# Kernel optimization log

Hardware: AMD Instinct MI355X
Metric: run time of the kernel (lower is better)

The kernel has to match this reference:

```python
import jax, jax.numpy as jnp
import numpy as np

N, E = 50000, 800000
NF, EF, S = 128, 64, 128

def _lin(key, fan_in, fan_out):
    k1, k2 = jax.random.split(key)
    lim = 1.0 / np.sqrt(fan_in)
    W = jax.random.uniform(k1, (fan_in, fan_out), jnp.float32, -lim, lim)
    b = jax.random.uniform(k2, (fan_out,), jnp.float32, -lim, lim)
    return W, b

def setup_inputs() -> dict:
    key = jax.random.key(0)
    ks = jax.random.split(key, 12)
    x = jax.random.normal(ks[0], (N, NF), jnp.float32)
    edge_index = jax.random.randint(ks[1], (2, E), 0, N, jnp.int64)
    edge_attr = jax.random.normal(ks[2], (E, EF), jnp.float32)
    Wn, bn = _lin(ks[3], NF, S)
    We, be = _lin(ks[4], EF, S)
    Wzc, bzc = _lin(ks[5], S, S)   # GCNConv weight/bias (z gate)
    Wzl, bzl = _lin(ks[6], 2 * S, S)
    Wrc, brc = _lin(ks[7], S, S)
    Wrl, brl = _lin(ks[8], 2 * S, S)
    Whc, bhc = _lin(ks[9], S, S)
    Whl, bhl = _lin(ks[10], 2 * S, S)
    Wout, bout = _lin(ks[11], 3 * S, 1)
    return dict(x=x, edge_index=edge_index, edge_attr=edge_attr,
                Wn=Wn, bn=bn, We=We, be=be,
                Wzc=Wzc, bzc=bzc, Wzl=Wzl, bzl=bzl,
                Wrc=Wrc, brc=brc, Wrl=Wrl, brl=brl,
                Whc=Whc, bhc=bhc, Whl=Whl, bhl=bhl,
                Wout=Wout, bout=bout)

def reference(x, edge_index, edge_attr, Wn, bn, We, be,
              Wzc, bzc, Wzl, bzl, Wrc, brc, Wrl, brl,
              Whc, bhc, Whl, bhl, Wout, bout):
    n = x.shape[0]
    src, dst = edge_index[0], edge_index[1]
    xe = jax.nn.relu(x @ Wn + bn)                      # [N,S]
    ea = jax.nn.relu(edge_attr @ We + be)              # [E,S]
    # GCNConv normalization with self-loops (shared across the 3 gates)
    loop = jnp.arange(n)
    s2 = jnp.concatenate([src, loop])
    d2 = jnp.concatenate([dst, loop])
    deg = jax.ops.segment_sum(jnp.ones(s2.shape[0], xe.dtype), d2, n)
    dinv = jax.lax.rsqrt(deg)                          # deg >= 1 (self loops)
    norm = (dinv[s2] * dinv[d2])[:, None]              # [E+N,1]
    def gcn(W, b):
        xw = xe @ W
        return jax.ops.segment_sum(xw[s2] * norm, d2, n) + b
    H = jnp.zeros_like(xe)
    Z = jax.nn.sigmoid(jnp.concatenate([gcn(Wzc, bzc), H], 1) @ Wzl + bzl)
    R = jax.nn.sigmoid(jnp.concatenate([gcn(Wrc, brc), H], 1) @ Wrl + brl)
    Ht = jnp.tanh(jnp.concatenate([gcn(Whc, bhc), H * R], 1) @ Whl + bhl)
    H = Z * H + (1.0 - Z) * Ht                          # [N,S]
    edge_h = jnp.concatenate([H[src], H[dst], ea], axis=1)  # [E,3S]
    return edge_h @ Wout + bout                         # [E,1]
```

## Files before the change

### kernel.cpp

```cpp
#include <hip/hip_runtime.h>
#include <hip/hip_bf16.h>
#include <math.h>

#define NN 50000
#define EE 800000

typedef __bf16 bf16x8 __attribute__((ext_vector_type(8)));
typedef float f32x4 __attribute__((ext_vector_type(4)));

__global__ void k_deg(const int* __restrict__ ei, int* __restrict__ deg) {
    int e = blockIdx.x * 256 + threadIdx.x;
    if (e < EE) atomicAdd(&deg[ei[EE + e]], 1);
}

__global__ void k_wprep(const float* __restrict__ Wzc, const float* __restrict__ bzc,
                        const float* __restrict__ Wzl, const float* __restrict__ bzl,
                        const float* __restrict__ Whc, const float* __restrict__ bhc,
                        const float* __restrict__ Whl, const float* __restrict__ bhl,
                        float* __restrict__ Wcat, float* __restrict__ cb) {
    int i = blockIdx.x;
    int k = threadIdx.x;
    float sz = 0.f, sh = 0.f;
    for (int j = 0; j < 128; j++) {
        sz += Wzc[i * 128 + j] * Wzl[j * 128 + k];
        sh += Whc[i * 128 + j] * Whl[j * 128 + k];
    }
    Wcat[i * 256 + 2 * k]     = sz;
    Wcat[i * 256 + 2 * k + 1] = sh;
    if (i == 0) {
        float bz = bzl[k], bh = bhl[k];
        for (int j = 0; j < 128; j++) {
            bz += bzc[j] * Wzl[j * 128 + k];
            bh += bhc[j] * Whl[j * 128 + k];
        }
        cb[2 * k]     = bz;
        cb[2 * k + 1] = bh;
    }
}

__global__ __launch_bounds__(256) void k_gemm1(const float* __restrict__ A,
                                               const float* __restrict__ B,
                                               const float* __restrict__ bias,
                                               const int* __restrict__ deg,
                                               __hip_bfloat16* __restrict__ C, int M) {
    __shared__ float As[8][128];
    __shared__ float Bs[8][128];
    const int m0 = blockIdx.x * 128;
    const int tid = threadIdx.x;
    const int tx = tid & 15;
    const int ty = tid >> 4;
    float acc[8][8];
#pragma unroll
    for (int i = 0; i < 8; i++)
#pragma unroll
        for (int j = 0; j < 8; j++) acc[i][j] = 0.f;

    for (int k0 = 0; k0 < 128; k0 += 8) {
        {
            int m = tid >> 1, kk = (tid & 1) * 4;
            float4 av = make_float4(0.f, 0.f, 0.f, 0.f);
            if (m0 + m < M) av = *(const float4*)&A[(size_t)(m0 + m) * 128 + k0 + kk];
            As[kk + 0][m] = av.x; As[kk + 1][m] = av.y;
            As[kk + 2][m] = av.z; As[kk + 3][m] = av.w;
        }
        {
            int kb = tid >> 5, n = (tid & 31) * 4;
            float4 bv = *(const float4*)&B[(size_t)(k0 + kb) * 128 + n];
            *(float4*)&Bs[kb][n] = bv;
        }
        __syncthreads();
#pragma unroll
        for (int kk = 0; kk < 8; kk++) {
            float af[8], bf[8];
#pragma unroll
            for (int i = 0; i < 8; i++) af[i] = As[kk][ty + 16 * i];
#pragma unroll
            for (int j = 0; j < 8; j++) bf[j] = Bs[kk][tx + 16 * j];
#pragma unroll
            for (int i = 0; i < 8; i++)
#pragma unroll
                for (int j = 0; j < 8; j++) acc[i][j] += af[i] * bf[j];
        }
        __syncthreads();
    }
#pragma unroll
    for (int i = 0; i < 8; i++) {
        int row = m0 + ty + 16 * i;
        if (row >= M) continue;
        float di = rsqrtf((float)(deg[row] + 1));
#pragma unroll
        for (int j = 0; j < 8; j++) {
            int cg = tx + 16 * j;
            float v = fmaxf(acc[i][j] + bias[cg], 0.f) * di;
            C[(size_t)row * 128 + cg] = __float2bfloat16(v);
        }
    }
}

__global__ __launch_bounds__(256) void k_gemm_gate(const float* __restrict__ A,
                                                   const float* __restrict__ B,
                                                   const float* __restrict__ cb,
                                                   const float* __restrict__ Wout,
                                                   float* __restrict__ aArr,
                                                   float* __restrict__ bArr, int M) {
    __shared__ float As[8][128];
    __shared__ float Bs[8][128];
    const int m0 = blockIdx.x * 128;
    const int n0 = blockIdx.y * 128;
    const int tid = threadIdx.x;
    const int tx = tid & 15;
    const int ty = tid >> 4;
    float acc[8][8];
#pragma unroll
    for (int i = 0; i < 8; i++)
#pragma unroll
        for (int j = 0; j < 8; j++) acc[i][j] = 0.f;

    for (int k0 = 0; k0 < 128; k0 += 8) {
        {
            int m = tid >> 1, kk = (tid & 1) * 4;
            float4 av = make_float4(0.f, 0.f, 0.f, 0.f);
            if (m0 + m < M) av = *(const float4*)&A[(size_t)(m0 + m) * 128 + k0 + kk];
            As[kk + 0][m] = av.x; As[kk + 1][m] = av.y;
            As[kk + 2][m] = av.z; As[kk + 3][m] = av.w;
        }
        {
            int kb = tid >> 5, n = (tid & 31) * 4;
            float4 bv = *(const float4*)&B[(size_t)(k0 + kb) * 256 + n0 + n];
            *(float4*)&Bs[kb][n] = bv;
        }
        __syncthreads();
#pragma unroll
        for (int kk = 0; kk < 8; kk++) {
            float af[8], bf[8];
#pragma unroll
            for (int i = 0; i < 8; i++) af[i] = As[kk][ty + 16 * i];
#pragma unroll
            for (int j = 0; j < 8; j++) bf[j] = Bs[kk][tx + 16 * j];
#pragma unroll
            for (int i = 0; i < 8; i++)
#pragma unroll
                for (int j = 0; j < 8; j++) acc[i][j] += af[i] * bf[j];
        }
        __syncthreads();
    }
#pragma unroll
    for (int i = 0; i < 8; i++) {
        int row = m0 + ty + 16 * i;
        bool live = (row < M);
        float pa = 0.f, pb = 0.f;
#pragma unroll
        for (int j = 0; j < 8; j++) {
            int col = n0 + tx + 16 * j;
            float val = acc[i][j] + cb[col];
            bool odd = (col & 1);
            float s = odd ? tanhf(val) : (1.f / (1.f + expf(-val)));
            float partner = __shfl_xor(s, 1);
            if (!odd) {
                int k = col >> 1;
                float h = (1.f - s) * partner;
                pa += h * Wout[k];
                pb += h * Wout[128 + k];
            }
        }
#pragma unroll
        for (int off = 1; off < 16; off <<= 1) {
            pa += __shfl_xor(pa, off);
            pb += __shfl_xor(pb, off);
        }
        if (live && tx == 0) {
            atomicAdd(&aArr[row], pa);
            atomicAdd(&bArr[row], pb);
        }
    }
}

__global__ void k_scan_a(const int* __restrict__ deg, int* __restrict__ partial) {
    __shared__ int s[256];
    int i = blockIdx.x * 256 + threadIdx.x;
    s[threadIdx.x] = (i < NN) ? deg[i] : 0;
    __syncthreads();
    for (int off = 128; off > 0; off >>= 1) {
        if (threadIdx.x < off) s[threadIdx.x] += s[threadIdx.x + off];
        __syncthreads();
    }
    if (threadIdx.x == 0) partial[blockIdx.x] = s[0];
}

__global__ void k_scan_b(const int* __restrict__ partial, int* __restrict__ partoff, int nb) {
    __shared__ int s[256];
    int v = (threadIdx.x < nb) ? partial[threadIdx.x] : 0;
    s[threadIdx.x] = v;
    __syncthreads();
    for (int off = 1; off < 256; off <<= 1) {
        int t = (threadIdx.x >= off) ? s[threadIdx.x - off] : 0;
        __syncthreads();
        s[threadIdx.x] += t;
        __syncthreads();
    }
    partoff[threadIdx.x] = s[threadIdx.x] - v;
}

__global__ void k_scan_c(const int* __restrict__ deg, const int* __restrict__ partoff,
                         int* __restrict__ rowptr, int* __restrict__ cursor) {
    __shared__ int s[256];
    int i = blockIdx.x * 256 + threadIdx.x;
    int v = (i < NN) ? deg[i] : 0;
    s[threadIdx.x] = v;
    __syncthreads();
    for (int off = 1; off < 256; off <<= 1) {
        int t = (threadIdx.x >= off) ? s[threadIdx.x - off] : 0;
        __syncthreads();
        s[threadIdx.x] += t;
        __syncthreads();
    }
    int excl = s[threadIdx.x] - v + partoff[blockIdx.x];
    if (i < NN) { rowptr[i] = excl; cursor[i] = excl; }
    if (i == 0) rowptr[NN] = EE;
}

__global__ void k_fill(const int* __restrict__ ei, int* __restrict__ cursor,
                       int* __restrict__ col) {
    int e = blockIdx.x * 256 + threadIdx.x;
    if (e < EE) {
        int d = ei[EE + e];
        int p = atomicAdd(&cursor[d], 1);
        col[p] = ei[e];
    }
}

__global__ __launch_bounds__(256) void k_gather(const unsigned int* __restrict__ xsu,
                                                const int* __restrict__ rowptr,
                                                const int* __restrict__ col,
                                                const int* __restrict__ deg,
                                                float* __restrict__ agg) {
    int gt = blockIdx.x * 256 + threadIdx.x;
    int node = gt >> 6;
    int lane = threadIdx.x & 63;
    if (node >= NN) return;
    int beg = rowptr[node], end = rowptr[node + 1];
    unsigned int u = xsu[(size_t)node * 64 + lane];
    float a0 = __uint_as_float(u << 16);
    float a1 = __uint_as_float(u & 0xFFFF0000u);
    int p = beg;
    while (p < end) {
        int rem = end - p;
        int chunk = rem < 64 ? rem : 64;
        int cv = (lane < chunk) ? col[p + lane] : 0;
        int j = 0;
        for (; j + 4 <= chunk; j += 4) {
            int s0 = __shfl(cv, j + 0);
            int s1 = __shfl(cv, j + 1);
            int s2 = __shfl(cv, j + 2);
            int s3 = __shfl(cv, j + 3);
            unsigned int u0 = xsu[(size_t)s0 * 64 + lane];
            unsigned int u1 = xsu[(size_t)s1 * 64 + lane];
            unsigned int u2 = xsu[(size_t)s2 * 64 + lane];
            unsigned int u3 = xsu[(size_t)s3 * 64 + lane];
            a0 += __uint_as_float(u0 << 16) + __uint_as_float(u1 << 16)
                + __uint_as_float(u2 << 16) + __uint_as_float(u3 << 16);
            a1 += __uint_as_float(u0 & 0xFFFF0000u) + __uint_as_float(u1 & 0xFFFF0000u)
                + __uint_as_float(u2 & 0xFFFF0000u) + __uint_as_float(u3 & 0xFFFF0000u);
        }
        for (; j < chunk; j++) {
            int s = __shfl(cv, j);
            unsigned int uv = xsu[(size_t)s * 64 + lane];
            a0 += __uint_as_float(uv << 16);
            a1 += __uint_as_float(uv & 0xFFFF0000u);
        }
        p += 64;
    }
    float di = rsqrtf((float)(deg[node] + 1));
    *(float2*)(agg + (size_t)node * 128 + lane * 2) = make_float2(a0 * di, a1 * di);
}

__global__ __launch_bounds__(256) void k_edge_mfma(const float* __restrict__ EA,
                                                   const int* __restrict__ ei,
                                                   const float* __restrict__ We,
                                                   const float* __restrict__ be,
                                                   const float* __restrict__ Wout,
                                                   const float* __restrict__ boutp,
                                                   const float* __restrict__ aArr,
                                                   const float* __restrict__ bArr,
                                                   float* __restrict__ out) {
    const int lane = threadIdx.x & 63;
    const int ln = lane & 15;
    const int q  = lane >> 4;
    const int wid = (blockIdx.x * 256 + threadIdx.x) >> 6;
    const int nw  = gridDim.x * 4;

    bf16x8 bfrag[2][8];
#pragma unroll
    for (int h = 0; h < 2; h++)
#pragma unroll
        for (int t = 0; t < 8; t++)
#pragma unroll
            for (int j = 0; j < 8; j++)
                bfrag[h][t][j] = (__bf16)We[(h * 32 + q * 8 + j) * 128 + t * 16 + ln];

    float beR[8], w3R[8];
#pragma unroll
    for (int t = 0; t < 8; t++) {
        beR[t] = be[t * 16 + ln];
        w3R[t] = Wout[256 + t * 16 + ln];
    }
    const float b0 = boutp[0];

    for (int tile = wid; tile < EE / 16; tile += nw) {
        const int e0 = tile * 16;
        const float* arow = EA + (size_t)(e0 + ln) * 64;
        float4 v0 = *(const float4*)(arow + q * 8);
        float4 v1 = *(const float4*)(arow + q * 8 + 4);
        float4 v2 = *(const float4*)(arow + 32 + q * 8);
        float4 v3 = *(const float4*)(arow + 32 + q * 8 + 4);
        bf16x8 af0, af1;
        af0[0] = (__bf16)v0.x; af0[1] = (__bf16)v0.y; af0[2] = (__bf16)v0.z; af0[3] = (__bf16)v0.w;
        af0[4] = (__bf16)v1.x; af0[5] = (__bf16)v1.y; af0[6] = (__bf16)v1.z; af0[7] = (__bf16)v1.w;
        af1[0] = (__bf16)v2.x; af1[1] = (__bf16)v2.y; af1[2] = (__bf16)v2.z; af1[3] = (__bf16)v2.w;
        af1[4] = (__bf16)v3.x; af1[5] = (__bf16)v3.y; af1[6] = (__bf16)v3.z; af1[7] = (__bf16)v3.w;

        f32x4 acc[8];
#pragma unroll
        for (int t = 0; t < 8; t++) acc[t] = (f32x4){0.f, 0.f, 0.f, 0.f};
#pragma unroll
        for (int t = 0; t < 8; t++)
            acc[t] = __builtin_amdgcn_mfma_f32_16x16x32_bf16(af0, bfrag[0][t], acc[t], 0, 0, 0);
#pragma unroll
        for (int t = 0; t < 8; t++)
            acc[t] = __builtin_amdgcn_mfma_f32_16x16x32_bf16(af1, bfrag[1][t], acc[t], 0, 0, 0);

        float part[4] = {0.f, 0.f, 0.f, 0.f};
#pragma unroll
        for (int t = 0; t < 8; t++)
#pragma unroll
            for (int r = 0; r < 4; r++) {
                float y = acc[t][r] + beR[t];
                y = fmaxf(y, 0.f);
                part[r] += y * w3R[t];
            }
#pragma unroll
        for (int off = 1; off < 16; off <<= 1) {
#pragma unroll
            for (int r = 0; r < 4; r++) part[r] += __shfl_xor(part[r], off);
        }
        if (ln < 4) {
            float c = (ln == 0) ? part[0] : (ln == 1) ? part[1] : (ln == 2) ? part[2] : part[3];
            int e = e0 + q * 4 + ln;
            out[e] = c + aArr[ei[e]] + bArr[ei[EE + e]] + b0;
        }
    }
}

extern "C" void kernel_launch(void* const* d_in, const int* in_sizes, int n_in,
                              void* d_out, int out_size, void* d_ws, size_t ws_size,
                              hipStream_t stream) {
    const float* x    = (const float*)d_in[0];
    const int*   ei   = (const int*)d_in[1];
    const float* ea   = (const float*)d_in[2];
    const float* Wn   = (const float*)d_in[3];
    const float* bn   = (const float*)d_in[4];
    const float* We   = (const float*)d_in[5];
    const float* be   = (const float*)d_in[6];
    const float* Wzc  = (const float*)d_in[7];
    const float* bzc  = (const float*)d_in[8];
    const float* Wzl  = (const float*)d_in[9];
    const float* bzl  = (const float*)d_in[10];
    const float* Whc  = (const float*)d_in[15];
    const float* bhc  = (const float*)d_in[16];
    const float* Whl  = (const float*)d_in[17];
    const float* bhl  = (const float*)d_in[18];
    const float* Wout = (const float*)d_in[19];
    const float* bout = (const float*)d_in[20];
    float* out = (float*)d_out;

    char* w = (char*)d_ws;
    auto carve = [&](size_t bytes) {
        void* p = (void*)w;
        w += (bytes + 255) / 256 * 256;
        return p;
    };
    __hip_bfloat16* xs = (__hip_bfloat16*)carve((size_t)NN * 128 * 2);
    float* agg     = (float*)carve((size_t)NN * 128 * 4);
    float* Wcat    = (float*)carve(128 * 256 * 4);
    float* cb      = (float*)carve(256 * 4);
    int*   deg     = (int*)carve((size_t)NN * 4);
    int*   rowptr  = (int*)carve((size_t)(NN + 1) * 4);
    int*   cursor  = (int*)carve((size_t)NN * 4);
    int*   col     = (int*)carve((size_t)EE * 4);
    int*   partial = (int*)carve(256 * 4);
    int*   partoff = (int*)carve(256 * 4);
    float* aArr    = (float*)carve((size_t)NN * 4);
    float* bArr    = (float*)carve((size_t)NN * 4);

    hipMemsetAsync(deg, 0, (size_t)NN * 4, stream);
    hipMemsetAsync(aArr, 0, (size_t)NN * 4, stream);
    hipMemsetAsync(bArr, 0, (size_t)NN * 4, stream);
    k_deg<<<(EE + 255) / 256, 256, 0, stream>>>(ei, deg);
    k_wprep<<<128, 128, 0, stream>>>(Wzc, bzc, Wzl, bzl, Whc, bhc, Whl, bhl, Wcat, cb);

    k_gemm1<<<dim3(391, 1), 256, 0, stream>>>(x, Wn, bn, deg, xs, NN);

    const int NB = (NN + 255) / 256;
    k_scan_a<<<NB, 256, 0, stream>>>(deg, partial);
    k_scan_b<<<1, 256, 0, stream>>>(partial, partoff, NB);
    k_scan_c<<<NB, 256, 0, stream>>>(deg, partoff, rowptr, cursor);
    k_fill<<<(EE + 255) / 256, 256, 0, stream>>>(ei, cursor, col);

    k_gather<<<(NN * 64 + 255) / 256, 256, 0, stream>>>((const unsigned int*)xs, rowptr, col, deg, agg);

    k_gemm_gate<<<dim3(391, 2), 256, 0, stream>>>(agg, Wcat, cb, Wout, aArr, bArr, NN);

    k_edge_mfma<<<2048, 256, 0, stream>>>(ea, ei, We, be, Wout, bout, aArr, bArr, out);
}
```

Before: 631.1 us.

## Replace FP32 SIMT GEMMs with bf16 MFMA kernels and store aggregate as bf16

Rewrites the node embedding GEMM and the gate GEMM as wave-level bf16 MFMA kernels that keep weight fragments in registers and loop over 16-row tiles. The gather kernel now writes its aggregate in packed bf16 rather than fp32, which halves that buffer's traffic and lets the gate kernel load MFMA operands directly. The goal is to cut the FP32 FMA cost of the two dense GEMMs, at the price of bf16 rounding on x and on the aggregated features.

```diff
diff --git a/kernel.cpp b/kernel.cpp
--- a/kernel.cpp
+++ b/kernel.cpp
@@ -7,6 +7,7 @@
 
 typedef __bf16 bf16x8 __attribute__((ext_vector_type(8)));
 typedef float f32x4 __attribute__((ext_vector_type(4)));
+typedef unsigned int u32x4 __attribute__((ext_vector_type(4)));
 
 __global__ void k_deg(const int* __restrict__ ei, int* __restrict__ deg) {
     int e = blockIdx.x * 256 + threadIdx.x;
@@ -38,139 +39,148 @@
     }
 }
 
-__global__ __launch_bounds__(256) void k_gemm1(const float* __restrict__ A,
-                                               const float* __restrict__ B,
-                                               const float* __restrict__ bias,
-                                               const int* __restrict__ deg,
-                                               __hip_bfloat16* __restrict__ C, int M) {
-    __shared__ float As[8][128];
-    __shared__ float Bs[8][128];
-    const int m0 = blockIdx.x * 128;
-    const int tid = threadIdx.x;
-    const int tx = tid & 15;
-    const int ty = tid >> 4;
-    float acc[8][8];
-#pragma unroll
-    for (int i = 0; i < 8; i++)
-#pragma unroll
-        for (int j = 0; j < 8; j++) acc[i][j] = 0.f;
-
-    for (int k0 = 0; k0 < 128; k0 += 8) {
-        {
-            int m = tid >> 1, kk = (tid & 1) * 4;
-            float4 av = make_float4(0.f, 0.f, 0.f, 0.f);
-            if (m0 + m < M) av = *(const float4*)&A[(size_t)(m0 + m) * 128 + k0 + kk];
-            As[kk + 0][m] = av.x; As[kk + 1][m] = av.y;
-            As[kk + 2][m] = av.z; As[kk + 3][m] = av.w;
-        }
-        {
-            int kb = tid >> 5, n = (tid & 31) * 4;
-            float4 bv = *(const float4*)&B[(size_t)(k0 + kb) * 128 + n];
-            *(float4*)&Bs[kb][n] = bv;
-        }
-        __syncthreads();
-#pragma unroll
-        for (int kk = 0; kk < 8; kk++) {
-            float af[8], bf[8];
-#pragma unroll
-            for (int i = 0; i < 8; i++) af[i] = As[kk][ty + 16 * i];
-#pragma unroll
-            for (int j = 0; j < 8; j++) bf[j] = Bs[kk][tx + 16 * j];
-#pragma unroll
-            for (int i = 0; i < 8; i++)
-#pragma unroll
-                for (int j = 0; j < 8; j++) acc[i][j] += af[i] * bf[j];
-        }
-        __syncthreads();
-    }
-#pragma unroll
-    for (int i = 0; i < 8; i++) {
-        int row = m0 + ty + 16 * i;
-        if (row >= M) continue;
-        float di = rsqrtf((float)(deg[row] + 1));
-#pragma unroll
-        for (int j = 0; j < 8; j++) {
-            int cg = tx + 16 * j;
-            float v = fmaxf(acc[i][j] + bias[cg], 0.f) * di;
-            C[(size_t)row * 128 + cg] = __float2bfloat16(v);
-        }
-    }
-}
-
-__global__ __launch_bounds__(256) void k_gemm_gate(const float* __restrict__ A,
-                                                   const float* __restrict__ B,
+__global__ __launch_bounds__(256) void k_g1_mfma(const float* __restrict__ x,
+                                                 const float* __restrict__ Wn,
+                                                 const float* __restrict__ bn,
+                                                 const int* __restrict__ deg,
+                                                 __hip_bfloat16* __restrict__ xs) {
+    const int lane = threadIdx.x & 63;
+    const int ln = lane & 15;
+    const int q  = lane >> 4;
+    const int wid = (blockIdx.x * 256 + threadIdx.x) >> 6;
+    const int nw  = gridDim.x * 4;
+    const int ch  = wid & 1;
+    const int step = nw >> 1;
+
+    bf16x8 bfrag[4][4];
+#pragma unroll
+    for (int t = 0; t < 4; t++)
+#pragma unroll
+        for (int kc = 0; kc < 4; kc++)
+#pragma unroll
+            for (int j = 0; j < 8; j++)
+                bfrag[t][kc][j] = (__bf16)Wn[(kc * 32 + q * 8 + j) * 128 + ch * 64 + t * 16 + ln];
+    float biasR[4];
+#pragma unroll
+    for (int t = 0; t < 4; t++) biasR[t] = bn[ch * 64 + t * 16 + ln];
+
+    for (int rt = wid >> 1; rt < 3125; rt += step) {
+        const int e0 = rt * 16;
+        const float* arow = x + (size_t)(e0 + ln) * 128;
+        bf16x8 af[4];
+#pragma unroll
+        for (int kc = 0; kc < 4; kc++) {
+            float4 v0 = *(const float4*)(arow + kc * 32 + q * 8);
+            float4 v1 = *(const float4*)(arow + kc * 32 + q * 8 + 4);
+            af[kc][0] = (__bf16)v0.x; af[kc][1] = (__bf16)v0.y;
+            af[kc][2] = (__bf16)v0.z; af[kc][3] = (__bf16)v0.w;
+            af[kc][4] = (__bf16)v1.x; af[kc][5] = (__bf16)v1.y;
+            af[kc][6] = (__bf16)v1.z; af[kc][7] = (__bf16)v1.w;
+        }
+        f32x4 acc[4];
+#pragma unroll
+        for (int t = 0; t < 4; t++) acc[t] = (f32x4){0.f, 0.f, 0.f, 0.f};
+#pragma unroll
+        for (int t = 0; t < 4; t++)
+#pragma unroll
+            for (int kc = 0; kc < 4; kc++)
+                acc[t] = __builtin_amdgcn_mfma_f32_16x16x32_bf16(af[kc], bfrag[t][kc], acc[t], 0, 0, 0);
+
+        float diR[4];
+#pragma unroll
+        for (int r = 0; r < 4; r++) diR[r] = rsqrtf((float)(deg[e0 + q * 4 + r] + 1));
+#pragma unroll
+        for (int t = 0; t < 4; t++)
+#pragma unroll
+            for (int r = 0; r < 4; r++) {
+                float v = fmaxf(acc[t][r] + biasR[t], 0.f) * diR[r];
+                xs[(size_t)(e0 + q * 4 + r) * 128 + ch * 64 + t * 16 + ln] = __float2bfloat16(v);
+            }
+    }
+}
+
+__global__ __launch_bounds__(256) void k_gate_mfma(const unsigned int* __restrict__ aggu,
+                                                   const float* __restrict__ Wcat,
                                                    const float* __restrict__ cb,
                                                    const float* __restrict__ Wout,
                                                    float* __restrict__ aArr,
-                                                   float* __restrict__ bArr, int M) {
-    __shared__ float As[8][128];
-    __shared__ float Bs[8][128];
-    const int m0 = blockIdx.x * 128;
-    const int n0 = blockIdx.y * 128;
-    const int tid = threadIdx.x;
-    const int tx = tid & 15;
-    const int ty = tid >> 4;
-    float acc[8][8];
-#pragma unroll
-    for (int i = 0; i < 8; i++)
-#pragma unroll
-        for (int j = 0; j < 8; j++) acc[i][j] = 0.f;
-
-    for (int k0 = 0; k0 < 128; k0 += 8) {
-        {
-            int m = tid >> 1, kk = (tid & 1) * 4;
-            float4 av = make_float4(0.f, 0.f, 0.f, 0.f);
-            if (m0 + m < M) av = *(const float4*)&A[(size_t)(m0 + m) * 128 + k0 + kk];
-            As[kk + 0][m] = av.x; As[kk + 1][m] = av.y;
-            As[kk + 2][m] = av.z; As[kk + 3][m] = av.w;
-        }
-        {
-            int kb = tid >> 5, n = (tid & 31) * 4;
-            float4 bv = *(const float4*)&B[(size_t)(k0 + kb) * 256 + n0 + n];
-            *(float4*)&Bs[kb][n] = bv;
-        }
-        __syncthreads();
-#pragma unroll
-        for (int kk = 0; kk < 8; kk++) {
-            float af[8], bf[8];
-#pragma unroll
-            for (int i = 0; i < 8; i++) af[i] = As[kk][ty + 16 * i];
-#pragma unroll
-            for (int j = 0; j < 8; j++) bf[j] = Bs[kk][tx + 16 * j];
-#pragma unroll
-            for (int i = 0; i < 8; i++)
-#pragma unroll
-                for (int j = 0; j < 8; j++) acc[i][j] += af[i] * bf[j];
-        }
-        __syncthreads();
-    }
-#pragma unroll
-    for (int i = 0; i < 8; i++) {
-        int row = m0 + ty + 16 * i;
-        bool live = (row < M);
-        float pa = 0.f, pb = 0.f;
-#pragma unroll
-        for (int j = 0; j < 8; j++) {
-            int col = n0 + tx + 16 * j;
-            float val = acc[i][j] + cb[col];
-            bool odd = (col & 1);
-            float s = odd ? tanhf(val) : (1.f / (1.f + expf(-val)));
-            float partner = __shfl_xor(s, 1);
-            if (!odd) {
-                int k = col >> 1;
-                float h = (1.f - s) * partner;
-                pa += h * Wout[k];
-                pb += h * Wout[128 + k];
+                                                   float* __restrict__ bArr) {
+    const int lane = threadIdx.x & 63;
+    const int ln = lane & 15;
+    const int q  = lane >> 4;
+    const int wid = (blockIdx.x * 256 + threadIdx.x) >> 6;
+    const int nw  = gridDim.x * 4;
+    const int cq  = wid & 3;
+    const int step = nw >> 2;
+
+    bf16x8 bfrag[4][4];
+#pragma unroll
+    for (int t = 0; t < 4; t++)
+#pragma unroll
+        for (int kc = 0; kc < 4; kc++)
+#pragma unroll
+            for (int j = 0; j < 8; j++)
+                bfrag[t][kc][j] = (__bf16)Wcat[(kc * 32 + q * 8 + j) * 256 + cq * 64 + t * 16 + ln];
+
+    float cbR[4], wAR[4], wBR[4];
+#pragma unroll
+    for (int t = 0; t < 4; t++) {
+        int col = cq * 64 + t * 16 + ln;
+        cbR[t] = cb[col];
+        int k = col >> 1;
+        wAR[t] = Wout[k];
+        wBR[t] = Wout[128 + k];
+    }
+    const bool odd = (ln & 1);
+
+    for (int rt = wid >> 2; rt < 3125; rt += step) {
+        const int e0 = rt * 16;
+        const u32x4* arow = (const u32x4*)aggu + (size_t)(e0 + ln) * 16;
+        bf16x8 af[4];
+#pragma unroll
+        for (int kc = 0; kc < 4; kc++) {
+            u32x4 uv = arow[kc * 4 + q];
+            af[kc] = __builtin_bit_cast(bf16x8, uv);
+        }
+        f32x4 acc[4];
+#pragma unroll
+        for (int t = 0; t < 4; t++) acc[t] = (f32x4){0.f, 0.f, 0.f, 0.f};
+#pragma unroll
+        for (int t = 0; t < 4; t++)
+#pragma unroll
+            for (int kc = 0; kc < 4; kc++)
+                acc[t] = __builtin_amdgcn_mfma_f32_16x16x32_bf16(af[kc], bfrag[t][kc], acc[t], 0, 0, 0);
+
+        float pa[4] = {0.f, 0.f, 0.f, 0.f};
+        float pb[4] = {0.f, 0.f, 0.f, 0.f};
+#pragma unroll
+        for (int t = 0; t < 4; t++)
+#pragma unroll
+            for (int r = 0; r < 4; r++) {
+                float val = acc[t][r] + cbR[t];
+                float s = odd ? tanhf(val) : (1.f / (1.f + expf(-val)));
+                float partner = __shfl_xor(s, 1);
+                if (!odd) {
+                    float h = (1.f - s) * partner;
+                    pa[r] += h * wAR[t];
+                    pb[r] += h * wBR[t];
+                }
             }
-        }
 #pragma unroll
         for (int off = 1; off < 16; off <<= 1) {
-            pa += __shfl_xor(pa, off);
-            pb += __shfl_xor(pb, off);
-        }
-        if (live && tx == 0) {
-            atomicAdd(&aArr[row], pa);
-            atomicAdd(&bArr[row], pb);
+#pragma unroll
+            for (int r = 0; r < 4; r++) {
+                pa[r] += __shfl_xor(pa[r], off);
+                pb[r] += __shfl_xor(pb[r], off);
+            }
+        }
+        if (ln < 4) {
+            float v = (ln == 0) ? pa[0] : (ln == 1) ? pa[1] : (ln == 2) ? pa[2] : pa[3];
+            atomicAdd(&aArr[e0 + q * 4 + ln], v);
+        } else if (ln < 8) {
+            int r = ln - 4;
+            float v = (r == 0) ? pb[0] : (r == 1) ? pb[1] : (r == 2) ? pb[2] : pb[3];
+            atomicAdd(&bArr[e0 + q * 4 + r], v);
         }
     }
 }
@@ -233,7 +243,7 @@
                                                 const int* __restrict__ rowptr,
                                                 const int* __restrict__ col,
                                                 const int* __restrict__ deg,
-                                                float* __restrict__ agg) {
+                                                unsigned int* __restrict__ aggu) {
     int gt = blockIdx.x * 256 + threadIdx.x;
     int node = gt >> 6;
     int lane = threadIdx.x & 63;
@@ -271,7 +281,11 @@
         p += 64;
     }
     float di = rsqrtf((float)(deg[node] + 1));
-    *(float2*)(agg + (size_t)node * 128 + lane * 2) = make_float2(a0 * di, a1 * di);
+    __hip_bfloat16 b0 = __float2bfloat16(a0 * di);
+    __hip_bfloat16 b1 = __float2bfloat16(a1 * di);
+    unsigned int lo = *(unsigned short*)&b0;
+    unsigned int hi = *(unsigned short*)&b1;
+    aggu[(size_t)node * 64 + lane] = lo | (hi << 16);
 }
 
 __global__ __launch_bounds__(256) void k_edge_mfma(const float* __restrict__ EA,
@@ -380,7 +394,7 @@
         return p;
     };
     __hip_bfloat16* xs = (__hip_bfloat16*)carve((size_t)NN * 128 * 2);
-    float* agg     = (float*)carve((size_t)NN * 128 * 4);
+    unsigned int* aggu = (unsigned int*)carve((size_t)NN * 64 * 4);
     float* Wcat    = (float*)carve(128 * 256 * 4);
     float* cb      = (float*)carve(256 * 4);
     int*   deg     = (int*)carve((size_t)NN * 4);
@@ -398,7 +412,7 @@
     k_deg<<<(EE + 255) / 256, 256, 0, stream>>>(ei, deg);
     k_wprep<<<128, 128, 0, stream>>>(Wzc, bzc, Wzl, bzl, Whc, bhc, Whl, bhl, Wcat, cb);
 
-    k_gemm1<<<dim3(391, 1), 256, 0, stream>>>(x, Wn, bn, deg, xs, NN);
+    k_g1_mfma<<<384, 256, 0, stream>>>(x, Wn, bn, deg, xs);
 
     const int NB = (NN + 255) / 256;
     k_scan_a<<<NB, 256, 0, stream>>>(deg, partial);
@@ -406,9 +420,9 @@
     k_scan_c<<<NB, 256, 0, stream>>>(deg, partoff, rowptr, cursor);
     k_fill<<<(EE + 255) / 256, 256, 0, stream>>>(ei, cursor, col);
 
-    k_gather<<<(NN * 64 + 255) / 256, 256, 0, stream>>>((const unsigned int*)xs, rowptr, col, deg, agg);
-
-    k_gemm_gate<<<dim3(391, 2), 256, 0, stream>>>(agg, Wcat, cb, Wout, aArr, bArr, NN);
+    k_gather<<<(NN * 64 + 255) / 256, 256, 0, stream>>>((const unsigned int*)xs, rowptr, col, deg, aggu);
+
+    k_gate_mfma<<<512, 256, 0, stream>>>(aggu, Wcat, cb, Wout, aArr, bArr);
 
     k_edge_mfma<<<2048, 256, 0, stream>>>(ea, ei, We, be, Wout, bout, aArr, bArr, out);
 }
```

Measured after the change: 544.1 us. 13.8% less time.
